# Kernel optimization log

Hardware: AMD Instinct MI355X
Metric: run time of the kernel (lower is better)

## Reference

```python
import jax, jax.numpy as jnp
import numpy as np
from jax import lax

# LiteMSA config: in_ch=256, out_ch=256, dim=8, heads=32, total_dim=256, scales=(3,)
DIM = 8
QKV_CH = 768          # 3 * total_dim
PW_GROUPS = 96        # 3 * heads


def setup_inputs() -> dict:
    key = jax.random.key(0)
    ks = jax.random.split(key, 5)
    x = jax.random.normal(ks[0], (16, 256, 64, 64), jnp.float32)
    w_qkv = jax.random.normal(ks[1], (768, 256), jnp.float32) * 0.02      # 1x1 conv
    w_dw = jax.random.normal(ks[2], (768, 1, 3, 3), jnp.float32) * 0.02   # depthwise 3x3
    w_pw = jax.random.normal(ks[3], (768, 8, 1, 1), jnp.float32) * 0.02   # grouped 1x1, 96 groups
    w_proj = jax.random.normal(ks[4], (256, 512), jnp.float32) * 0.02     # 1x1 conv
    bn_gamma = jnp.ones((256,), jnp.float32)
    bn_beta = jnp.zeros((256,), jnp.float32)
    bn_mean = jnp.zeros((256,), jnp.float32)
    bn_var = jnp.ones((256,), jnp.float32)
    return {"x": x, "w_qkv": w_qkv, "w_dw": w_dw, "w_pw": w_pw, "w_proj": w_proj,
            "bn_gamma": bn_gamma, "bn_beta": bn_beta, "bn_mean": bn_mean, "bn_var": bn_var}


def reference(x, w_qkv, w_dw, w_pw, w_proj, bn_gamma, bn_beta, bn_mean, bn_var):
    B, _, H, W = x.shape
    dn = ("NCHW", "OIHW", "NCHW")
    # qkv 1x1 conv
    qkv = jnp.einsum("bchw,oc->bohw", x, w_qkv)  # [B,768,H,W]
    # multi-scale aggregation: depthwise 3x3 -> grouped 1x1
    agg = lax.conv_general_dilated(qkv, w_dw, (1, 1), "SAME",
                                   dimension_numbers=dn, feature_group_count=QKV_CH)
    agg = lax.conv_general_dilated(agg, w_pw, (1, 1), "SAME",
                                   dimension_numbers=dn, feature_group_count=PW_GROUPS)
    ms = jnp.concatenate([qkv, agg], axis=1)  # [B,1536,H,W]
    # [B, heads_total=64, N=H*W, 3*dim]
    ms = ms.reshape(B, -1, 3 * DIM, H * W).transpose(0, 1, 3, 2)
    q = jax.nn.relu(ms[..., :DIM])
    k = jax.nn.relu(ms[..., DIM:2 * DIM])
    v = ms[..., 2 * DIM:]
    # pad v with ones for normalizer channel
    v = jnp.concatenate([v, jnp.ones(v.shape[:-1] + (1,), v.dtype)], axis=-1)  # [B,h,N,dim+1]
    kv = jnp.einsum("bhnd,bhne->bhde", k, v)   # [B,h,dim,dim+1]
    out = jnp.einsum("bhnd,bhde->bhne", q, kv)  # [B,h,N,dim+1]
    out = out[..., :DIM] / (out[..., DIM:] + 1e-15)
    out = out.transpose(0, 1, 3, 2).reshape(B, -1, H, W)  # [B,512,H,W]
    # proj 1x1 conv + BatchNorm (inference, running stats)
    y = jnp.einsum("bchw,oc->bohw", out, w_proj)
    inv = bn_gamma / jnp.sqrt(bn_var + 1e-5)
    y = y * inv[None, :, None, None] + (bn_beta - bn_mean * inv)[None, :, None, None]
    return y
```

## Files before the change

kernel.cpp:

```cpp
#include <hip/hip_runtime.h>
#include <hip/hip_bf16.h>


#define NB 16
#define CQKV 768
#define P4096 4096
#define QFIX_CAP (1u << 21)

typedef __bf16 bf16x8 __attribute__((ext_vector_type(8)));
typedef float f32x4 __attribute__((ext_vector_type(4)));

#define MFMA_BF16 __builtin_amdgcn_mfma_f32_16x16x32_bf16

__device__ __forceinline__ ushort f2bf(float f) {
    union { float f; unsigned int u; } x; x.f = f;
    unsigned int u = x.u;
    unsigned int r = (u + 0x7FFFu + ((u >> 16) & 1u)) >> 16;
    return (ushort)r;
}
__device__ __forceinline__ float bf2f(ushort u) {
    union { unsigned int u; float f; } x; x.u = ((unsigned int)u) << 16;
    return x.f;
}
__device__ __forceinline__ unsigned int pk2bf(float x, float y) {
    __hip_bfloat162 h = __float22bfloat162_rn(make_float2(x, y));
    union { __hip_bfloat162 b; unsigned int u; } c; c.b = h; return c.u;
}

__device__ __forceinline__ void gload16(void* lds, const void* g) {
    __builtin_amdgcn_global_load_lds(
        (const __attribute__((address_space(1))) void*)g,
        (__attribute__((address_space(3))) void*)lds, 16, 0, 0);
}

__global__ __launch_bounds__(128) void conv_w(
    const float* __restrict__ W, ushort* __restrict__ Ah, ushort* __restrict__ Al,
    unsigned int* __restrict__ qmeta)
{
    const int rv = blockIdx.x;
    const int t  = threadIdx.x;
    if (rv == 0 && t == 0) qmeta[0] = 0;
    int phys;
    if (rv < 256) phys = (rv >> 3) * 24 + (rv & 7);
    else { int r2 = rv - 256; phys = (r2 >> 4) * 24 + 8 + (r2 & 15); }
    int c = t * 2;
    float w0 = W[(size_t)phys * 256 + c];
    float w1 = W[(size_t)phys * 256 + c + 1];
    unsigned int h = pk2bf(w0, w1);
    float f0 = __uint_as_float(h << 16);
    float f1 = __uint_as_float(h & 0xffff0000u);
    unsigned int l = pk2bf(w0 - f0, w1 - f1);
    int sl = ((c >> 3) & 3) ^ ((rv >> 1) & 3);
    int idx = (c & ~31) + sl * 8 + (c & 7);
    *(unsigned int*)&Ah[(size_t)rv * 256 + idx] = h;
    *(unsigned int*)&Al[(size_t)rv * 256 + idx] = l;
}

__global__ __launch_bounds__(256) void conv_wp(
    const float* __restrict__ W, ushort* __restrict__ Awp)
{
    const int m = blockIdx.x;
    const int t = threadIdx.x;
    int c = t * 2;
    float w0 = W[(size_t)m * 512 + c];
    float w1 = W[(size_t)m * 512 + c + 1];
    unsigned int h = pk2bf(w0, w1);
    int sl = ((c >> 3) & 3) ^ ((m >> 1) & 3);
    int idx = (c & ~31) + sl * 8 + (c & 7);
    *(unsigned int*)&Awp[(size_t)m * 512 + idx] = h;
}

__global__ __launch_bounds__(256) void conv_x(
    const float* __restrict__ X, ushort* __restrict__ XTh, ushort* __restrict__ XTl)
{
    const int pt = blockIdx.x;
    const int ct = blockIdx.y;
    const int b  = blockIdx.z;
    const int t  = threadIdx.x;
    const int p0 = pt * 64, c0 = ct * 64;

    __shared__ float tile[64][65];

    {
        int cr = t >> 2, pc = (t & 3) * 16;
        const float* xr = X + ((size_t)b * 256 + c0 + cr) * P4096 + p0 + pc;
        float4 v0 = *(const float4*)xr;
        float4 v1 = *(const float4*)(xr + 4);
        float4 v2 = *(const float4*)(xr + 8);
        float4 v3 = *(const float4*)(xr + 12);
        float* d = &tile[cr][pc];
        d[0]=v0.x; d[1]=v0.y; d[2]=v0.z; d[3]=v0.w;
        d[4]=v1.x; d[5]=v1.y; d[6]=v1.z; d[7]=v1.w;
        d[8]=v2.x; d[9]=v2.y; d[10]=v2.z; d[11]=v2.w;
        d[12]=v3.x; d[13]=v3.y; d[14]=v3.z; d[15]=v3.w;
    }
    __syncthreads();

    #pragma unroll
    for (int pass = 0; pass < 2; pass++) {
        int tp = t >> 2;
        int cc = (t & 3) + pass * 4;
        int p  = p0 + tp;
        float v[8];
        #pragma unroll
        for (int j = 0; j < 8; j++) v[j] = tile[cc * 8 + j][tp];
        union { unsigned int u[4]; uint4 q; } H, L;
        #pragma unroll
        for (int i = 0; i < 4; i++) {
            unsigned int h = pk2bf(v[2 * i], v[2 * i + 1]);
            H.u[i] = h;
            float f0 = __uint_as_float(h << 16);
            float f1 = __uint_as_float(h & 0xffff0000u);
            L.u[i] = pk2bf(v[2 * i] - f0, v[2 * i + 1] - f1);
        }
        int c = c0 + cc * 8;
        int sl = ((c >> 3) & 3) ^ ((p >> 1) & 3);
        size_t idx = ((size_t)b * P4096 + p) * 256 + (c & ~31) + sl * 8;
        *(uint4*)&XTh[idx] = H.q;
        *(uint4*)&XTl[idx] = L.q;
    }
}

__global__ __launch_bounds__(256, 3) void gemm_fused(
    const ushort* __restrict__ Ah, const ushort* __restrict__ Al,
    const ushort* __restrict__ Bh, const ushort* __restrict__ Bl,
    ushort* __restrict__ Cbf, float* __restrict__ qplane,
    unsigned int* __restrict__ qmeta)
{
    const int hw = blockIdx.x;
    const int lg = (hw & 7) * 384 + (hw >> 3);
    const int mt = lg % 6;
    const int rem = lg / 6;
    const int n0 = (rem & 31) * 128;
    const int b  = rem >> 5;
    const int t  = threadIdx.x;
    const int wave = t >> 6, lane = t & 63, quad = lane >> 4, l15 = lane & 15;
    const int wr = wave >> 1, wc = wave & 1;
    const int M0 = mt * 128;

    __shared__ __align__(16) char smem[49152];

    int aoff[4], boff[4];
    #pragma unroll
    for (int i = 0; i < 4; i++) {
        int ra = wr * 64 + i * 16 + l15;
        aoff[i] = ra * 64 + ((quad ^ ((ra >> 1) & 3)) << 4);
        int rb = wc * 64 + i * 16 + l15;
        boff[i] = rb * 64 + ((quad ^ ((rb >> 1) & 3)) << 4);
    }

    const int srow = t >> 2;
    const int schunk = (t & 3) * 8;
    const size_t abase = (size_t)(M0 + srow) * 256 + schunk;
    const size_t bbase = ((size_t)b * P4096 + n0 + srow) * 256 + schunk;
    const int ldsoff = wave * 1024;

    f32x4 acc[4][4];
    #pragma unroll
    for (int mi = 0; mi < 4; mi++)
        #pragma unroll
        for (int nj = 0; nj < 4; nj++)
            #pragma unroll
            for (int r = 0; r < 4; r++) acc[mi][nj][r] = 0.0f;

    if (mt < 2) {
        char* AsH = smem;
        char* AsL = smem + 8192;
        char* BsH[2] = { smem + 16384, smem + 24576 };
        char* BsL[2] = { smem + 32768, smem + 40960 };

        auto stageA = [&](int kw) {
            #pragma unroll
            for (int i = 0; i < 2; i++) {
                int lo = ldsoff + i * 4096;
                size_t so = (size_t)(i * 64) * 256 + (size_t)kw * 32;
                gload16(AsH + lo, Ah + abase + so);
                gload16(AsL + lo, Al + abase + so);
            }
        };
        auto stageB = [&](int d, int kw) {
            #pragma unroll
            for (int i = 0; i < 2; i++) {
                int lo = ldsoff + i * 4096;
                size_t so = (size_t)(i * 64) * 256 + (size_t)kw * 32;
                gload16(BsH[d] + lo, Bh + bbase + so);
                gload16(BsL[d] + lo, Bl + bbase + so);
            }
        };
        stageA(0); stageB(0, 0);
        for (int kw = 0; kw < 8; kw++) {
            int cur = kw & 1;
            asm volatile("s_waitcnt vmcnt(0)" ::: "memory");
            __builtin_amdgcn_s_barrier();
            bf16x8 ah[4], al[4];
            #pragma unroll
            for (int mi = 0; mi < 4; mi++) {
                ah[mi] = *(const bf16x8*)(AsH + aoff[mi]);
                al[mi] = *(const bf16x8*)(AsL + aoff[mi]);
            }
            asm volatile("s_waitcnt lgkmcnt(0)" ::: "memory");
            __builtin_amdgcn_sched_barrier(0);
            __builtin_amdgcn_s_barrier();
            if (kw < 7) { stageA(kw + 1); stageB(cur ^ 1, kw + 1); }
            #pragma unroll
            for (int nj = 0; nj < 4; nj++) {
                bf16x8 bh = *(const bf16x8*)(BsH[cur] + boff[nj]);
                bf16x8 bl = *(const bf16x8*)(BsL[cur] + boff[nj]);
                #pragma unroll
                for (int mi = 0; mi < 4; mi++) {
                    acc[mi][nj] = MFMA_BF16(ah[mi], bh, acc[mi][nj], 0, 0, 0);
                    acc[mi][nj] = MFMA_BF16(al[mi], bh, acc[mi][nj], 0, 0, 0);
                    acc[mi][nj] = MFMA_BF16(ah[mi], bl, acc[mi][nj], 0, 0, 0);
                }
            }
        }
        unsigned int* qlist = qmeta + 16;
        #pragma unroll
        for (int mi = 0; mi < 4; mi++)
            #pragma unroll
            for (int nj = 0; nj < 4; nj++)
                #pragma unroll
                for (int r = 0; r < 4; r++) {
                    int rv = M0 + wr * 64 + mi * 16 + quad * 4 + r;
                    int rp = (rv >> 3) * 24 + (rv & 7);
                    int col = n0 + wc * 64 + nj * 16 + l15;
                    float v = acc[mi][nj][r];
                    Cbf[((size_t)b * CQKV + rp) * P4096 + col] = f2bf(v);
                    qplane[((size_t)b * 256 + rv) * P4096 + col] = v;
                    if (fabsf(v) < 1e-4f) {
                        unsigned int idx = atomicAdd(qmeta, 1u);
                        if (idx < QFIX_CAP)
                            qlist[idx] = (unsigned int)(((b * 256 + rv) << 12) | col);
                    }
                }
    } else {
        char* As[3] = { smem, smem + 8192, smem + 16384 };
        char* Bs[3] = { smem + 24576, smem + 32768, smem + 40960 };
        auto stageKV = [&](int d, int kw) {
            #pragma unroll
            for (int i = 0; i < 2; i++) {
                int lo = ldsoff + i * 4096;
                size_t so = (size_t)(i * 64) * 256 + (size_t)kw * 32;
                gload16(As[d] + lo, Ah + abase + so);
                gload16(Bs[d] + lo, Bh + bbase + so);
            }
        };
        stageKV(0, 0);
        stageKV(1, 1);
        #pragma unroll
        for (int kw = 0; kw < 8; kw++) {
            int cur = kw % 3;
            if (kw < 6) {
                stageKV((kw + 2) % 3, kw + 2);
                asm volatile("s_waitcnt vmcnt(8)" ::: "memory");
            } else if (kw == 6) {
                asm volatile("s_waitcnt vmcnt(4)" ::: "memory");
            } else {
                asm volatile("s_waitcnt vmcnt(0)" ::: "memory");
            }
            __builtin_amdgcn_s_barrier();
            bf16x8 ah[4];
            #pragma unroll
            for (int mi = 0; mi < 4; mi++)
                ah[mi] = *(const bf16x8*)(As[cur] + aoff[mi]);
            #pragma unroll
            for (int nj = 0; nj < 4; nj++) {
                bf16x8 bh = *(const bf16x8*)(Bs[cur] + boff[nj]);
                #pragma unroll
                for (int mi = 0; mi < 4; mi++)
                    acc[mi][nj] = MFMA_BF16(ah[mi], bh, acc[mi][nj], 0, 0, 0);
            }
            __builtin_amdgcn_s_barrier();
        }
        #pragma unroll
        for (int mi = 0; mi < 4; mi++)
            #pragma unroll
            for (int nj = 0; nj < 4; nj++)
                #pragma unroll
                for (int r = 0; r < 4; r++) {
                    int rv2 = (M0 - 256) + wr * 64 + mi * 16 + quad * 4 + r;
                    int rp = (rv2 >> 4) * 24 + 8 + (rv2 & 15);
                    int col = n0 + wc * 64 + nj * 16 + l15;
                    Cbf[((size_t)b * CQKV + rp) * P4096 + col] = f2bf(acc[mi][nj][r]);
                }
    }
}

__global__ __launch_bounds__(256) void qfix2_kernel(
    float* __restrict__ qplane, const float* __restrict__ w_qkv,
    const float* __restrict__ x, const unsigned int* __restrict__ qmeta)
{
    unsigned int n = qmeta[0];
    if (n > QFIX_CAP) n = QFIX_CAP;
    const unsigned int* list = qmeta + 16;
    const int wave = threadIdx.x >> 6, lane = threadIdx.x & 63;
    for (unsigned int e = blockIdx.x * 4 + wave; e < n; e += gridDim.x * 4) {
        unsigned int i = list[e];
        int p   = (int)(i & 4095);
        int qch = (int)((i >> 12) & 255);
        int b   = (int)(i >> 20);
        int row = (qch >> 3) * 24 + (qch & 7);
        const float* wr = w_qkv + (size_t)row * 256;
        const float* xr = x + (size_t)b * 256 * P4096 + p;
        double s = 0.0;
        #pragma unroll
        for (int j = 0; j < 4; j++) {
            int c = lane * 4 + j;
            s += (double)wr[c] * (double)xr[(size_t)c * P4096];
        }
        #pragma unroll
        for (int off = 32; off > 0; off >>= 1) s += __shfl_xor(s, off, 64);
        if (lane == 0)
            qplane[((size_t)(b * 256 + qch)) * P4096 + p] = (float)s;
    }
}

__global__ __launch_bounds__(512, 8) void dwpw_kernel(
    const ushort* __restrict__ qkv, const float* __restrict__ wdw,
    const float* __restrict__ wpw, ushort* __restrict__ agg)
{
    const int rt = blockIdx.x;
    const int g  = blockIdx.y;
    const int b  = blockIdx.z;
    const int t  = threadIdx.x;
    const int r0 = rt * 16;
    const int cg = g * 8;

    __shared__ __align__(16) ushort tile[8][18][80];

    const ushort* src = qkv + ((size_t)(b * CQKV + cg)) * P4096;

    if (t < 288) {
        int ch = t / 36;
        int rr = (t % 36) >> 1;
        int side = t & 1;
        *(uint4*)&tile[ch][rr][side * 72] = make_uint4(0, 0, 0, 0);
    }
    #pragma unroll
    for (int i = 0; i < 3; i++) {
        int id = t + i * 512;
        if (id < 1152) {
            int ch  = id / 144;
            int rem = id - ch * 144;
            int rr  = rem >> 3;
            int oct = (rem & 7) * 8;
            int grow = r0 - 1 + rr;
            uint4 v = make_uint4(0, 0, 0, 0);
            if (grow >= 0 && grow < 64)
                v = *(const uint4*)(src + (size_t)ch * P4096 + (size_t)grow * 64 + oct);
            *(uint4*)&tile[ch][rr][8 + oct] = v;
        }
    }
    __syncthreads();

    const int kc  = t & 31;
    const int row = t >> 5;
    const float* wdwg = wdw + (size_t)cg * 9;
    const float* wpwg = wpw + (size_t)cg * 8;

    float acc0[8], acc1[8];
    #pragma unroll
    for (int oi = 0; oi < 8; oi++) { acc0[oi] = 0.0f; acc1[oi] = 0.0f; }

    #pragma unroll
    for (int c = 0; c < 8; c++) {
        float dv0 = 0.0f, dv1 = 0.0f;
        #pragma unroll
        for (int dy = 0; dy < 3; dy++) {
            const ushort* rp = &tile[c][row + dy][2 * kc + 4];
            unsigned int u1 = *(const unsigned int*)(rp + 2);
            unsigned int u2 = *(const unsigned int*)(rp + 4);
            unsigned int u3 = *(const unsigned int*)(rp + 6);
            float xm1 = __uint_as_float(u1 & 0xffff0000u);
            float x0  = __uint_as_float(u2 << 16);
            float x1  = __uint_as_float(u2 & 0xffff0000u);
            float x2  = __uint_as_float(u3 << 16);
            float w0 = wdwg[c * 9 + dy * 3 + 0];
            float w1 = wdwg[c * 9 + dy * 3 + 1];
            float w2 = wdwg[c * 9 + dy * 3 + 2];
            dv0 = fmaf(w0, xm1, dv0); dv0 = fmaf(w1, x0, dv0); dv0 = fmaf(w2, x1, dv0);
            dv1 = fmaf(w0, x0,  dv1); dv1 = fmaf(w1, x1, dv1); dv1 = fmaf(w2, x2, dv1);
        }
        #pragma unroll
        for (int oi = 0; oi < 8; oi++) {
            float w = wpwg[oi * 8 + c];
            acc0[oi] = fmaf(w, dv0, acc0[oi]);
            acc1[oi] = fmaf(w, dv1, acc1[oi]);
        }
    }

    size_t obase = ((size_t)(b * CQKV + cg)) * P4096 + (size_t)(r0 + row) * 64 + 2 * kc;
    #pragma unroll
    for (int oi = 0; oi < 8; oi++) {
        unsigned int u = (unsigned int)f2bf(acc0[oi]) |
                         ((unsigned int)f2bf(acc1[oi]) << 16);
        *(unsigned int*)&agg[obase + (size_t)oi * P4096] = u;
    }
}

__global__ __launch_bounds__(256) void kv_kernel(
    const ushort* __restrict__ qkv, const ushort* __restrict__ agg,
    float* __restrict__ kv)
{
    const int h = blockIdx.x, b = blockIdx.y, t = threadIdx.x;
    const ushort* src = (h < 32)
        ? qkv + ((size_t)(b * CQKV + h * 24)) * P4096
        : agg + ((size_t)(b * CQKV + (h - 32) * 24)) * P4096;

    float acc[72];
    #pragma unroll
    for (int i = 0; i < 72; i++) acc[i] = 0.0f;

    for (int pi = 0; pi < 16; pi++) {
        int p = t + pi * 256;
        float kvv[8], vv[8];
        #pragma unroll
        for (int d = 0; d < 8; d++) {
            float xk = bf2f(src[(size_t)(8 + d) * P4096 + p]);
            kvv[d] = xk > 0.0f ? xk : 0.0f;
        }
        #pragma unroll
        for (int e = 0; e < 8; e++) vv[e] = bf2f(src[(size_t)(16 + e) * P4096 + p]);
        #pragma unroll
        for (int d = 0; d < 8; d++) {
            #pragma unroll
            for (int e = 0; e < 8; e++) acc[d * 9 + e] += kvv[d] * vv[e];
            acc[d * 9 + 8] += kvv[d];
        }
    }

    #pragma unroll
    for (int i = 0; i < 72; i++) {
        float v = acc[i];
        #pragma unroll
        for (int off = 32; off > 0; off >>= 1) v += __shfl_xor(v, off, 64);
        acc[i] = v;
    }
    __shared__ float part[4][72];
    int wave = t >> 6, lane = t & 63;
    if (lane == 0) {
        #pragma unroll
        for (int i = 0; i < 72; i++) part[wave][i] = acc[i];
    }
    __syncthreads();
    if (t < 72)
        kv[((size_t)b * 64 + h) * 72 + t] = part[0][t] + part[1][t] + part[2][t] + part[3][t];
}

__global__ __launch_bounds__(256) void attn_out_kernel(
    const float* __restrict__ qplane, ushort* __restrict__ agg,
    const float* __restrict__ kv)
{
    const int pt = blockIdx.x, h = blockIdx.y, b = blockIdx.z, t = threadIdx.x;
    __shared__ float kvs[72];
    if (t < 72) kvs[t] = kv[((size_t)b * 64 + h) * 72 + t];
    __syncthreads();

    const bool lohead = (h < 32);
    const float* srcf = lohead
        ? qplane + ((size_t)(b * 256 + h * 8)) * P4096 : nullptr;
    const ushort* srcb = lohead ? nullptr
        : agg + ((size_t)(b * CQKV + (h - 32) * 24)) * P4096;

    int p = pt * 512 + t * 2;
    float num0[8], num1[8]; float den0 = 0.0f, den1 = 0.0f;
    #pragma unroll
    for (int e = 0; e < 8; e++) { num0[e] = 0.0f; num1[e] = 0.0f; }
    #pragma unroll
    for (int d = 0; d < 8; d++) {
        float q0, q1;
        if (lohead) {
            float2 qq = *(const float2*)(srcf + (size_t)d * P4096 + p);
            q0 = qq.x; q1 = qq.y;
        } else {
            unsigned int u = *(const unsigned int*)(srcb + (size_t)d * P4096 + p);
            q0 = bf2f((ushort)(u & 0xffff)); q1 = bf2f((ushort)(u >> 16));
        }
        q0 = q0 > 0.0f ? q0 : 0.0f;
        q1 = q1 > 0.0f ? q1 : 0.0f;
        #pragma unroll
        for (int e = 0; e < 8; e++) {
            num0[e] += q0 * kvs[d * 9 + e];
            num1[e] += q1 * kvs[d * 9 + e];
        }
        den0 += q0 * kvs[d * 9 + 8];
        den1 += q1 * kvs[d * 9 + 8];
    }
    float rd0 = 1.0f / (den0 + 1e-15f);
    float rd1 = 1.0f / (den1 + 1e-15f);
    ushort* dst = agg + ((size_t)(b * CQKV + (h / 2) * 24 + 8 + (h % 2) * 8)) * P4096 + p;
    #pragma unroll
    for (int e = 0; e < 8; e++) {
        unsigned int u = (unsigned int)f2bf(num0[e] * rd0) |
                         ((unsigned int)f2bf(num1[e] * rd1) << 16);
        *(unsigned int*)(dst + (size_t)e * P4096) = u;
    }
}

__global__ __launch_bounds__(256, 3) void gemm_proj(
    const ushort* __restrict__ Awp,
    const ushort* __restrict__ Bagg,
    float* __restrict__ Y,
    const float* __restrict__ bn_g, const float* __restrict__ bn_b,
    const float* __restrict__ bn_m, const float* __restrict__ bn_v)
{
    const int hw = blockIdx.x;
    const int lg = (hw & 7) * 128 + (hw >> 3);
    const int mt = lg & 1;
    const int rem = lg >> 1;
    const int n0 = (rem & 31) * 128;
    const int b  = rem >> 5;
    const int t  = threadIdx.x;
    const int wave = t >> 6, lane = t & 63, quad = lane >> 4, l15 = lane & 15;
    const int wr = wave >> 1, wc = wave & 1;
    const int M0 = mt * 128;

    __shared__ __align__(16) ushort As[2][4096];
    __shared__ __align__(16) ushort Bs[2][5120];

    int aoff[4], boff[4];
    #pragma unroll
    for (int i = 0; i < 4; i++) {
        int ra = wr * 64 + i * 16 + l15;
        aoff[i] = ra * 64 + ((quad ^ ((ra >> 1) & 3)) << 4);
        int rb = wc * 64 + i * 16 + l15;
        boff[i] = rb * 80 + quad * 16;
    }

    const int arow0 = t >> 2, achk = (t & 3) * 8;
    const size_t abase = (size_t)(M0 + arow0) * 512 + achk;
    const size_t abase1 = (size_t)(M0 + 64 + arow0) * 512 + achk;
    const int ldsoffA = wave * 1024;

    const int bn_ = t & 127, half = t >> 7;
    const size_t bchanstride = (size_t)P4096;

    f32x4 acc[4][4];
    #pragma unroll
    for (int mi = 0; mi < 4; mi++)
        #pragma unroll
        for (int nj = 0; nj < 4; nj++)
            #pragma unroll
            for (int r = 0; r < 4; r++) acc[mi][nj][r] = 0.0f;

    auto stageA = [&](int d, int kw) {
        gload16((char*)As[d] + ldsoffA,        Awp + abase  + (size_t)kw * 32);
        gload16((char*)As[d] + ldsoffA + 4096, Awp + abase1 + (size_t)kw * 32);
    };
    ushort bu[16];
    auto loadB = [&](int kw) {
        const ushort* bsrc = Bagg
            + ((size_t)b * CQKV + (size_t)(kw * 2 + half) * 24 + 8) * P4096
            + n0 + bn_;
        #pragma unroll
        for (int j = 0; j < 16; j++) bu[j] = bsrc[(size_t)j * bchanstride];
    };
    auto writeB = [&](int d) {
        union { ushort us[8]; uint4 q; } P0, P1;
        #pragma unroll
        for (int j = 0; j < 8; j++) { P0.us[j] = bu[j]; P1.us[j] = bu[8 + j]; }
        ushort* dst = &Bs[d][bn_ * 40 + half * 16];
        *(uint4*)dst = P0.q;
        *(uint4*)(dst + 8) = P1.q;
    };

    stageA(0, 0);
    loadB(0);
    asm volatile("s_waitcnt vmcnt(0)" ::: "memory");
    writeB(0);
    asm volatile("s_waitcnt lgkmcnt(0)" ::: "memory");
    __builtin_amdgcn_s_barrier();

    for (int kw = 0; kw < 16; kw++) {
        int cur = kw & 1;
        if (kw < 15) {
            stageA(cur ^ 1, kw + 1);
            loadB(kw + 1);
        }
        bf16x8 af[4];
        #pragma unroll
        for (int mi = 0; mi < 4; mi++)
            af[mi] = *(const bf16x8*)((const char*)As[cur] + aoff[mi]);
        #pragma unroll
        for (int nj = 0; nj < 4; nj++) {
            bf16x8 bf = *(const bf16x8*)((const char*)Bs[cur] + boff[nj]);
            #pragma unroll
            for (int mi = 0; mi < 4; mi++)
                acc[mi][nj] = MFMA_BF16(af[mi], bf, acc[mi][nj], 0, 0, 0);
        }
        __builtin_amdgcn_s_barrier();
        if (kw < 15) {
            asm volatile("s_waitcnt vmcnt(0)" ::: "memory");
            writeB(cur ^ 1);
            asm volatile("s_waitcnt lgkmcnt(0)" ::: "memory");
        }
        __builtin_amdgcn_s_barrier();
    }

    #pragma unroll
    for (int mi = 0; mi < 4; mi++)
        #pragma unroll
        for (int nj = 0; nj < 4; nj++)
            #pragma unroll
            for (int r = 0; r < 4; r++) {
                int row = M0 + wr * 64 + mi * 16 + quad * 4 + r;
                int col = n0 + wc * 64 + nj * 16 + l15;
                float inv = bn_g[row] / sqrtf(bn_v[row] + 1e-5f);
                float v = acc[mi][nj][r] * inv + (bn_b[row] - bn_m[row] * inv);
                Y[((size_t)b * 256 + row) * P4096 + col] = v;
            }
}

extern "C" void kernel_launch(void* const* d_in, const int* in_sizes, int n_in,
                              void* d_out, int out_size, void* d_ws, size_t ws_size,
                              hipStream_t stream) {
    const float* x      = (const float*)d_in[0];
    const float* w_qkv  = (const float*)d_in[1];
    const float* w_dw   = (const float*)d_in[2];
    const float* w_pw   = (const float*)d_in[3];
    const float* w_proj = (const float*)d_in[4];
    const float* bn_g   = (const float*)d_in[5];
    const float* bn_b   = (const float*)d_in[6];
    const float* bn_m   = (const float*)d_in[7];
    const float* bn_v   = (const float*)d_in[8];
    float* y = (float*)d_out;

    char* ws = (char*)d_ws;
    ushort* qkv_bf = (ushort*)(ws);
    float*  qplane = (float*) (ws + 100663296);
    ushort* agg_bf = (ushort*)(ws + 167772160);
    ushort* XTh = (ushort*)(ws + 167772160);
    ushort* XTl = (ushort*)(ws + 167772160 + 33554432);
    ushort* Awh = (ushort*)(ws + 167772160 + 67108864);
    ushort* Awl = (ushort*)(ws + 167772160 + 67108864 + 393216);
    ushort* Awp = (ushort*)(ws + 100663296);
    float*  kvbuf  = (float*)d_out;
    unsigned int* qmeta = (unsigned int*)((char*)d_out + 524288);

    conv_w<<<dim3(768), 128, 0, stream>>>(w_qkv, Awh, Awl, qmeta);
    conv_x<<<dim3(64, 4, NB), 256, 0, stream>>>(x, XTh, XTl);

    gemm_fused<<<dim3(3072), 256, 0, stream>>>(
        Awh, Awl, XTh, XTl, qkv_bf, qplane, qmeta);

    qfix2_kernel<<<dim3(1024), 256, 0, stream>>>(qplane, w_qkv, x, qmeta);

    dwpw_kernel<<<dim3(4, 96, NB), 512, 0, stream>>>(qkv_bf, w_dw, w_pw, agg_bf);

    kv_kernel<<<dim3(64, NB), 256, 0, stream>>>(qkv_bf, agg_bf, kvbuf);

    attn_out_kernel<<<dim3(8, 64, NB), 256, 0, stream>>>(qplane, agg_bf, kvbuf);

    conv_wp<<<dim3(256), 256, 0, stream>>>(w_proj, Awp);

    gemm_proj<<<dim3(1024), 256, 0, stream>>>(
        Awp, agg_bf, y, bn_g, bn_b, bn_m, bn_v);
}
```

Baseline: 385.1 us.

## Fuse attention output computation into projection GEMM B-operand staging

Removes the separate attn_out kernel. The projection GEMM now loads q directly, applies ReLU and the per-head kv matrix held in shared memory, normalizes, and writes bf16 B tiles itself. The kv results and bf16 projection weights are placed in dead K-channel planes of the qkv buffer, so the agg attention-output writes and their re-read are avoided. The cost is more per-tile ALU work, 18KB of extra LDS for kv, occupancy hint lowered to 2, and each N-tile block redoing the attention math for both M tiles.

Result: slower. 416.5 us (+8.2%).

```diff
diff --git a/kernel.cpp b/kernel.cpp
--- a/kernel.cpp
+++ b/kernel.cpp
@@ -31,6 +31,13 @@
     __builtin_amdgcn_global_load_lds(
         (const __attribute__((address_space(1))) void*)g,
         (__attribute__((address_space(3))) void*)lds, 16, 0, 0);
+}
+
+__device__ __forceinline__ float* kvslot(const ushort* qkv, unsigned int f) {
+    unsigned int byte = f * 4u;
+    unsigned int plane = byte >> 13, within = byte & 8191u;
+    unsigned int ch = (plane >> 3) * 24u + (plane & 7u);
+    return (float*)((char*)qkv + ((size_t)ch << 13) + within);
 }
 
 __global__ __launch_bounds__(128) void conv_w(
@@ -57,7 +64,7 @@
 }
 
 __global__ __launch_bounds__(256) void conv_wp(
-    const float* __restrict__ W, ushort* __restrict__ Awp)
+    const float* __restrict__ W, ushort* __restrict__ qkvbuf)
 {
     const int m = blockIdx.x;
     const int t = threadIdx.x;
@@ -67,7 +74,9 @@
     unsigned int h = pk2bf(w0, w1);
     int sl = ((c >> 3) & 3) ^ ((m >> 1) & 3);
     int idx = (c & ~31) + sl * 8 + (c & 7);
-    *(unsigned int*)&Awp[(size_t)m * 512 + idx] = h;
+    ushort* dst = qkvbuf + (m >= 128 ? (size_t)32 * 4096 + (size_t)(m - 128) * 512
+                                     : (size_t)8 * 4096 + (size_t)m * 512);
+    *(unsigned int*)&dst[idx] = h;
 }
 
 __global__ __launch_bounds__(256) void conv_x(
@@ -400,7 +409,7 @@
 
 __global__ __launch_bounds__(256) void kv_kernel(
     const ushort* __restrict__ qkv, const ushort* __restrict__ agg,
-    float* __restrict__ kv)
+    ushort* __restrict__ kvdst)
 {
     const int h = blockIdx.x, b = blockIdx.y, t = threadIdx.x;
     const ushort* src = (h < 32)
@@ -444,62 +453,14 @@
     }
     __syncthreads();
     if (t < 72)
-        kv[((size_t)b * 64 + h) * 72 + t] = part[0][t] + part[1][t] + part[2][t] + part[3][t];
-}
-
-__global__ __launch_bounds__(256) void attn_out_kernel(
-    const float* __restrict__ qplane, ushort* __restrict__ agg,
-    const float* __restrict__ kv)
-{
-    const int pt = blockIdx.x, h = blockIdx.y, b = blockIdx.z, t = threadIdx.x;
-    __shared__ float kvs[72];
-    if (t < 72) kvs[t] = kv[((size_t)b * 64 + h) * 72 + t];
-    __syncthreads();
-
-    const bool lohead = (h < 32);
-    const float* srcf = lohead
-        ? qplane + ((size_t)(b * 256 + h * 8)) * P4096 : nullptr;
-    const ushort* srcb = lohead ? nullptr
-        : agg + ((size_t)(b * CQKV + (h - 32) * 24)) * P4096;
-
-    int p = pt * 512 + t * 2;
-    float num0[8], num1[8]; float den0 = 0.0f, den1 = 0.0f;
-    #pragma unroll
-    for (int e = 0; e < 8; e++) { num0[e] = 0.0f; num1[e] = 0.0f; }
-    #pragma unroll
-    for (int d = 0; d < 8; d++) {
-        float q0, q1;
-        if (lohead) {
-            float2 qq = *(const float2*)(srcf + (size_t)d * P4096 + p);
-            q0 = qq.x; q1 = qq.y;
-        } else {
-            unsigned int u = *(const unsigned int*)(srcb + (size_t)d * P4096 + p);
-            q0 = bf2f((ushort)(u & 0xffff)); q1 = bf2f((ushort)(u >> 16));
-        }
-        q0 = q0 > 0.0f ? q0 : 0.0f;
-        q1 = q1 > 0.0f ? q1 : 0.0f;
-        #pragma unroll
-        for (int e = 0; e < 8; e++) {
-            num0[e] += q0 * kvs[d * 9 + e];
-            num1[e] += q1 * kvs[d * 9 + e];
-        }
-        den0 += q0 * kvs[d * 9 + 8];
-        den1 += q1 * kvs[d * 9 + 8];
-    }
-    float rd0 = 1.0f / (den0 + 1e-15f);
-    float rd1 = 1.0f / (den1 + 1e-15f);
-    ushort* dst = agg + ((size_t)(b * CQKV + (h / 2) * 24 + 8 + (h % 2) * 8)) * P4096 + p;
-    #pragma unroll
-    for (int e = 0; e < 8; e++) {
-        unsigned int u = (unsigned int)f2bf(num0[e] * rd0) |
-                         ((unsigned int)f2bf(num1[e] * rd1) << 16);
-        *(unsigned int*)(dst + (size_t)e * P4096) = u;
-    }
-}
-
-__global__ __launch_bounds__(256, 3) void gemm_proj(
-    const ushort* __restrict__ Awp,
-    const ushort* __restrict__ Bagg,
+        *kvslot(kvdst, (unsigned int)(b * 64 + h) * 72u + t) =
+            part[0][t] + part[1][t] + part[2][t] + part[3][t];
+}
+
+__global__ __launch_bounds__(256, 2) void gemm_proj(
+    const ushort* __restrict__ qkv,
+    const ushort* __restrict__ agg,
+    const float* __restrict__ qplane,
     float* __restrict__ Y,
     const float* __restrict__ bn_g, const float* __restrict__ bn_b,
     const float* __restrict__ bn_m, const float* __restrict__ bn_v)
@@ -517,6 +478,7 @@
 
     __shared__ __align__(16) ushort As[2][4096];
     __shared__ __align__(16) ushort Bs[2][5120];
+    __shared__ float kvs[64][72];
 
     int aoff[4], boff[4];
     #pragma unroll
@@ -527,13 +489,17 @@
         boff[i] = rb * 80 + quad * 16;
     }
 
+    const ushort* AwpC = qkv + (mt ? (size_t)32 * 4096 : (size_t)8 * 4096);
     const int arow0 = t >> 2, achk = (t & 3) * 8;
-    const size_t abase = (size_t)(M0 + arow0) * 512 + achk;
-    const size_t abase1 = (size_t)(M0 + 64 + arow0) * 512 + achk;
+    const size_t abase  = (size_t)arow0 * 512 + achk;
+    const size_t abase1 = (size_t)(64 + arow0) * 512 + achk;
     const int ldsoffA = wave * 1024;
 
     const int bn_ = t & 127, half = t >> 7;
-    const size_t bchanstride = (size_t)P4096;
+    const int px = n0 + bn_;
+
+    for (int i = t; i < 4608; i += 256)
+        kvs[i / 72][i % 72] = *kvslot(qkv, (unsigned int)b * 4608u + i);
 
     f32x4 acc[4][4];
     #pragma unroll
@@ -544,16 +510,47 @@
             for (int r = 0; r < 4; r++) acc[mi][nj][r] = 0.0f;
 
     auto stageA = [&](int d, int kw) {
-        gload16((char*)As[d] + ldsoffA,        Awp + abase  + (size_t)kw * 32);
-        gload16((char*)As[d] + ldsoffA + 4096, Awp + abase1 + (size_t)kw * 32);
+        gload16((char*)As[d] + ldsoffA,        AwpC + abase  + (size_t)kw * 32);
+        gload16((char*)As[d] + ldsoffA + 4096, AwpC + abase1 + (size_t)kw * 32);
+    };
+    float qreg[2][8];
+    auto loadQ = [&](int kw) {
+        int hd0 = kw * 4 + half * 2;
+        #pragma unroll
+        for (int hh = 0; hh < 2; hh++) {
+            int hd = hd0 + hh;
+            if (hd < 32) {
+                #pragma unroll
+                for (int d = 0; d < 8; d++)
+                    qreg[hh][d] = qplane[((size_t)(b * 256 + hd * 8 + d)) * P4096 + px];
+            } else {
+                #pragma unroll
+                for (int d = 0; d < 8; d++)
+                    qreg[hh][d] = bf2f(agg[((size_t)(b * CQKV + (hd - 32) * 24 + d)) * P4096 + px]);
+            }
+        }
     };
     ushort bu[16];
-    auto loadB = [&](int kw) {
-        const ushort* bsrc = Bagg
-            + ((size_t)b * CQKV + (size_t)(kw * 2 + half) * 24 + 8) * P4096
-            + n0 + bn_;
-        #pragma unroll
-        for (int j = 0; j < 16; j++) bu[j] = bsrc[(size_t)j * bchanstride];
+    auto computeB = [&](int kw) {
+        int hd0 = kw * 4 + half * 2;
+        #pragma unroll
+        for (int hh = 0; hh < 2; hh++) {
+            int hd = hd0 + hh;
+            float num[8]; float den = 0.0f;
+            #pragma unroll
+            for (int e = 0; e < 8; e++) num[e] = 0.0f;
+            #pragma unroll
+            for (int d = 0; d < 8; d++) {
+                float q = qreg[hh][d];
+                q = q > 0.0f ? q : 0.0f;
+                #pragma unroll
+                for (int e = 0; e < 8; e++) num[e] += q * kvs[hd][d * 9 + e];
+                den += q * kvs[hd][d * 9 + 8];
+            }
+            float rd = 1.0f / (den + 1e-15f);
+            #pragma unroll
+            for (int e = 0; e < 8; e++) bu[hh * 8 + e] = f2bf(num[e] * rd);
+        }
     };
     auto writeB = [&](int d) {
         union { ushort us[8]; uint4 q; } P0, P1;
@@ -565,8 +562,9 @@
     };
 
     stageA(0, 0);
-    loadB(0);
-    asm volatile("s_waitcnt vmcnt(0)" ::: "memory");
+    loadQ(0);
+    __syncthreads();
+    computeB(0);
     writeB(0);
     asm volatile("s_waitcnt lgkmcnt(0)" ::: "memory");
     __builtin_amdgcn_s_barrier();
@@ -575,7 +573,7 @@
         int cur = kw & 1;
         if (kw < 15) {
             stageA(cur ^ 1, kw + 1);
-            loadB(kw + 1);
+            loadQ(kw + 1);
         }
         bf16x8 af[4];
         #pragma unroll
@@ -591,6 +589,7 @@
         __builtin_amdgcn_s_barrier();
         if (kw < 15) {
             asm volatile("s_waitcnt vmcnt(0)" ::: "memory");
+            computeB(kw + 1);
             writeB(cur ^ 1);
             asm volatile("s_waitcnt lgkmcnt(0)" ::: "memory");
         }
@@ -633,8 +632,6 @@
     ushort* XTl = (ushort*)(ws + 167772160 + 33554432);
     ushort* Awh = (ushort*)(ws + 167772160 + 67108864);
     ushort* Awl = (ushort*)(ws + 167772160 + 67108864 + 393216);
-    ushort* Awp = (ushort*)(ws + 100663296);
-    float*  kvbuf  = (float*)d_out;
     unsigned int* qmeta = (unsigned int*)((char*)d_out + 524288);
 
     conv_w<<<dim3(768), 128, 0, stream>>>(w_qkv, Awh, Awl, qmeta);
@@ -647,12 +644,10 @@
 
     dwpw_kernel<<<dim3(4, 96, NB), 512, 0, stream>>>(qkv_bf, w_dw, w_pw, agg_bf);
 
-    kv_kernel<<<dim3(64, NB), 256, 0, stream>>>(qkv_bf, agg_bf, kvbuf);
-
-    attn_out_kernel<<<dim3(8, 64, NB), 256, 0, stream>>>(qplane, agg_bf, kvbuf);
-
-    conv_wp<<<dim3(256), 256, 0, stream>>>(w_proj, Awp);
+    kv_kernel<<<dim3(64, NB), 256, 0, stream>>>(qkv_bf, agg_bf, qkv_bf);
+
+    conv_wp<<<dim3(256), 256, 0, stream>>>(w_proj, qkv_bf);
 
     gemm_proj<<<dim3(1024), 256, 0, stream>>>(
-        Awp, agg_bf, y, bn_g, bn_b, bn_m, bn_v);
-}
+        qkv_bf, agg_bf, qplane, y, bn_g, bn_b, bn_m, bn_v);
+}
```
